# Performance work log

Measured on AMD Instinct MI355X. Metric: run time of the kernel, lower is better.

The kernel has to match this reference:

```python
import math
import jax, jax.numpy as jnp
import numpy as np

B, N, D, H, HID = 2, 2048, 1024, 16, 4096
KS = (7, 25, 49)

def _alibi_slopes(n):
    def p2(m):
        start = 2.0 ** (-(2.0 ** (-(math.log2(m) - 3))))
        return [start * (start ** i) for i in range(m)]
    if math.log2(n).is_integer():
        s = p2(n)
    else:
        cp2 = 2 ** int(math.floor(math.log2(n)))
        s = p2(cp2) + p2(2 * cp2)[0::2][: n - cp2]
    return jnp.asarray(s, dtype=jnp.float32)

def _ln(x, g, b, eps=1e-5):
    m = x.mean(-1, keepdims=True)
    v = ((x - m) ** 2).mean(-1, keepdims=True)
    return (x - m) / jnp.sqrt(v + eps) * g + b

def _dwconv(x, w, pl, pr, mode, bias=None):
    # x: (B, D, L) channels-first, w: (D, 1, k) depthwise kernel
    xp = jnp.pad(x, ((0, 0), (0, 0), (pl, pr)), mode=mode)
    y = jax.lax.conv_general_dilated(xp, w, (1,), 'VALID',
                                     dimension_numbers=('NCH', 'OIH', 'NCH'),
                                     feature_group_count=x.shape[1])
    if bias is not None:
        y = y + bias[None, :, None]
    return y

def _forward(x, periodic_bias, alpha, dw7, dw25, dw49, ln1_g, ln1_b, ln2_g, ln2_b,
             Wq, bq, Wk, bk, Wv, bv, Wo, bo, W1, b1, W2, b2, tw, tb):
    Bx, Nx, Dm = x.shape
    hd = Dm // H
    # --- series decomposition: softmax-weighted multi-scale moving averages ---
    xt = x.transpose(0, 2, 1)  # (B, D, N)
    branches = [_dwconv(xt, w, k // 2, k // 2, 'reflect')
                for w, k in ((dw7, 7), (dw25, 25), (dw49, 49))]
    wmix = jax.nn.softmax(alpha)
    T = sum(br * wi for br, wi in zip(branches, wmix)).transpose(0, 2, 1)  # trend (B,N,D)
    S = x - T  # seasonal
    # --- ALiBi self-attention on normalized seasonal part ---
    sn = _ln(S, ln1_g, ln1_b)
    q = (jnp.einsum('bnd,ed->bne', sn, Wq) + bq).reshape(Bx, Nx, H, hd)
    k = (jnp.einsum('bnd,ed->bne', sn, Wk) + bk).reshape(Bx, Nx, H, hd)
    v = (jnp.einsum('bnd,ed->bne', sn, Wv) + bv).reshape(Bx, Nx, H, hd)
    logits = jnp.einsum('bqhd,bkhd->bhqk', q, k) / np.float32(np.sqrt(hd))
    idx = jnp.arange(Nx)
    dist = jnp.maximum(idx[None, :] - idx[:, None], 0).astype(jnp.float32)  # clamp(j-i, 0)
    slopes = _alibi_slopes(H)
    logits = logits - slopes[None, :, None, None] * dist[None, None] + periodic_bias[None, None]
    attn = jax.nn.softmax(logits, axis=-1)
    o = jnp.einsum('bhqk,bkhd->bqhd', attn, v).reshape(Bx, Nx, Dm)
    y = jnp.einsum('bnd,ed->bne', o, Wo) + bo
    x_s = S + y
    # --- dense FFN (exact GELU, as torch nn.GELU default) ---
    h = _ln(x_s, ln2_g, ln2_b)
    ffn = jnp.einsum('bnh,dh->bnd',
                     jax.nn.gelu(jnp.einsum('bnd,hd->bnh', h, W1) + b1, approximate=False),
                     W2) + b2
    x_s = x_s + ffn
    # --- trend path: depthwise conv k=5, zero padding 2 ---
    t_out = _dwconv(T.transpose(0, 2, 1), tw, 2, 2, 'constant', tb).transpose(0, 2, 1)
    return x_s + t_out

def setup_inputs():
    key = jax.random.key(0)
    ks = jax.random.split(key, 12)
    def lin(k, o, i):
        return jax.random.normal(k, (o, i), jnp.float32) / np.float32(np.sqrt(i))
    return {
        'x': jax.random.normal(ks[0], (B, N, D), jnp.float32),
        'periodic_bias': 0.1 * jax.random.normal(ks[1], (N, N), jnp.float32),
        'alpha': jnp.zeros((len(KS),), jnp.float32),
        'dw7': jnp.full((D, 1, 7), 1.0 / 7, jnp.float32),
        'dw25': jnp.full((D, 1, 25), 1.0 / 25, jnp.float32),
        'dw49': jnp.full((D, 1, 49), 1.0 / 49, jnp.float32),
        'ln1_g': jnp.ones((D,), jnp.float32), 'ln1_b': jnp.zeros((D,), jnp.float32),
        'ln2_g': jnp.ones((D,), jnp.float32), 'ln2_b': jnp.zeros((D,), jnp.float32),
        'Wq': lin(ks[2], D, D), 'bq': jnp.zeros((D,), jnp.float32),
        'Wk': lin(ks[3], D, D), 'bk': jnp.zeros((D,), jnp.float32),
        'Wv': lin(ks[4], D, D), 'bv': jnp.zeros((D,), jnp.float32),
        'Wo': lin(ks[5], D, D), 'bo': jnp.zeros((D,), jnp.float32),
        'W1': lin(ks[6], HID, D), 'b1': jnp.zeros((HID,), jnp.float32),
        'W2': lin(ks[7], D, HID), 'b2': jnp.zeros((D,), jnp.float32),
        'tw': 0.1 * jax.random.normal(ks[8], (D, 1, 5), jnp.float32),
        'tb': jnp.zeros((D,), jnp.float32),
    }

def reference(x, periodic_bias, alpha, dw7, dw25, dw49, ln1_g, ln1_b, ln2_g, ln2_b,
              Wq, bq, Wk, bk, Wv, bv, Wo, bo, W1, b1, W2, b2, tw, tb):
    out = _forward(x, periodic_bias, alpha, dw7, dw25, dw49, ln1_g, ln1_b, ln2_g, ln2_b,
                   Wq, bq, Wk, bk, Wv, bv, Wo, bo, W1, b1, W2, b2, tw, tb)
    return (out, jnp.zeros((), out.dtype))
```

## Files before the change

kernel.cpp:

```cpp
#include <hip/hip_runtime.h>
#include <cstdint>

#define BB 2
#define NN 2048
#define DD 1024
#define HH 16
#define HD 64
#define HID_ 4096
#define MM (BB*NN)

typedef __bf16 bf16x8 __attribute__((ext_vector_type(8)));
typedef float  f32x4  __attribute__((ext_vector_type(4)));

__device__ inline void gload_lds16(const void* g, void* l) {
  __builtin_amdgcn_global_load_lds((const __attribute__((address_space(1))) char*)g,
                                   (__attribute__((address_space(3))) char*)l, 16, 0, 0);
}
__device__ inline float max3f(float a, float b, float c) { return fmaxf(fmaxf(a, b), c); }

__global__ void k_wcomb(const float* __restrict__ alpha, const float* __restrict__ dw7,
                        const float* __restrict__ dw25, const float* __restrict__ dw49,
                        float* __restrict__ wc,
                        const float* __restrict__ bq, const float* __restrict__ bk,
                        const float* __restrict__ bv, float* __restrict__ b3) {
  int t = blockIdx.x;
  if (t == 49) {
    for (int i = threadIdx.x; i < 3 * DD; i += blockDim.x) {
      const float* s = (i < DD) ? bq : (i < 2 * DD ? bk : bv);
      b3[i] = s[i & (DD - 1)];
    }
    return;
  }
  float a0 = alpha[0], a1 = alpha[1], a2 = alpha[2];
  float mx = fmaxf(a0, fmaxf(a1, a2));
  float e0 = __expf(a0 - mx), e1 = __expf(a1 - mx), e2 = __expf(a2 - mx);
  float inv = 1.f / (e0 + e1 + e2);
  float w0 = e0 * inv, w1 = e1 * inv, w2 = e2 * inv;
  for (int d = threadIdx.x; d < DD; d += blockDim.x) {
    float v = w2 * dw49[d * 49 + t];
    if (t >= 12 && t <= 36) v += w1 * dw25[d * 25 + (t - 12)];
    if (t >= 21 && t <= 27) v += w0 * dw7[d * 7 + (t - 21)];
    wc[t * DD + d] = v;
  }
}

__global__ __launch_bounds__(256) void k_cvtall(const float* __restrict__ Wq, const float* __restrict__ Wk,
                         const float* __restrict__ Wv, const float* __restrict__ Wo,
                         const float* __restrict__ W1, const float* __restrict__ W2,
                         __bf16* __restrict__ dst) {
  size_t i = ((size_t)blockIdx.x * 256 + threadIdx.x) * 4;
  const float* s;
  if (i < 1048576u) s = Wq + i;
  else if (i < 2097152u) s = Wk + (i - 1048576u);
  else if (i < 3145728u) s = Wv + (i - 2097152u);
  else if (i < 4194304u) s = Wo + (i - 3145728u);
  else if (i < 8388608u) s = W1 + (i - 4194304u);
  else s = W2 + (i - 8388608u);
  float4 v = *(const float4*)s;
  dst[i] = (__bf16)v.x; dst[i+1] = (__bf16)v.y; dst[i+2] = (__bf16)v.z; dst[i+3] = (__bf16)v.w;
}

__global__ __launch_bounds__(256) void k_pbt(const float* __restrict__ pb,
                                             __bf16* __restrict__ pbt) {
  int q = blockIdx.x;
  int qt16 = q >> 4, qm = q & 15;
  for (int k = threadIdx.x; k < NN; k += 256) {
    float v = pb[(size_t)q * NN + k] * 1.4426950408889634f;
    int kt = k >> 4, g = (k >> 2) & 3, rr = k & 3;
    pbt[((size_t)qt16 * 128 + kt) * 256 + (qm + 16 * g) * 4 + rr] = (__bf16)v;
  }
}

__global__ __launch_bounds__(256) void k_decomp(const float* __restrict__ x,
                                                const float* __restrict__ wc,
                                                const float* __restrict__ tw,
                                                const float* __restrict__ tb,
                                                float* __restrict__ S,
                                                float* __restrict__ tout) {
  int bid = blockIdx.x;
  int db = bid & 3, ns = (bid >> 2) & 127, b = bid >> 9;
  int d = db * 256 + threadIdx.x;
  int n0 = ns * 16;
  const float* xb = x + (size_t)b * NN * DD + d;
  float xw[68];
#pragma unroll
  for (int i = 0; i < 68; ++i) {
    int n = n0 - 26 + i;
    n = (n < 0) ? -n : n;
    n = (n > NN - 1) ? 2 * (NN - 1) - n : n;
    xw[i] = xb[(size_t)n * DD];
  }
  float Tx[20];
#pragma unroll
  for (int j = 0; j < 20; ++j) Tx[j] = 0.f;
#pragma unroll
  for (int t = 0; t < 49; ++t) {
    float wv = wc[t * DD + d];
#pragma unroll
    for (int j = 0; j < 20; ++j) Tx[j] = fmaf(wv, xw[j + t], Tx[j]);
  }
#pragma unroll
  for (int j = 0; j < 20; ++j) {
    int row = n0 - 2 + j;
    if (row < 0 || row >= NN) Tx[j] = 0.f;
  }
  float tw5[5];
#pragma unroll
  for (int t = 0; t < 5; ++t) tw5[t] = tw[d * 5 + t];
  float tbv = tb[d];
  size_t base = ((size_t)b * NN + n0) * DD + d;
#pragma unroll
  for (int i = 0; i < 16; ++i) {
    S[base + (size_t)i * DD] = xw[i + 26] - Tx[i + 2];
    float acc = tbv;
#pragma unroll
    for (int t = 0; t < 5; ++t) acc = fmaf(tw5[t], Tx[i + t], acc);
    tout[base + (size_t)i * DD] = acc;
  }
}

__global__ __launch_bounds__(256) void k_ln(const float* __restrict__ x,
                                            const float* __restrict__ g,
                                            const float* __restrict__ bt,
                                            __bf16* __restrict__ y) {
  int row = blockIdx.x;
  const float* xr = x + (size_t)row * DD;
  int i = threadIdx.x * 4;
  float4 v = *(const float4*)&xr[i];
  float s = v.x + v.y + v.z + v.w;
  float sq = v.x * v.x + v.y * v.y + v.z * v.z + v.w * v.w;
#pragma unroll
  for (int m = 1; m <= 32; m <<= 1) { s += __shfl_xor(s, m); sq += __shfl_xor(sq, m); }
  __shared__ float rs[4], rq[4];
  int wid = threadIdx.x >> 6;
  if ((threadIdx.x & 63) == 0) { rs[wid] = s; rq[wid] = sq; }
  __syncthreads();
  s = rs[0] + rs[1] + rs[2] + rs[3];
  sq = rq[0] + rq[1] + rq[2] + rq[3];
  float mean = s * (1.f / DD);
  float var = sq * (1.f / DD) - mean * mean;
  float rstd = rsqrtf(var + 1e-5f);
  float4 gv = *(const float4*)&g[i];
  float4 bv = *(const float4*)&bt[i];
  __bf16* yr = y + (size_t)row * DD + i;
  yr[0] = (__bf16)((v.x - mean) * rstd * gv.x + bv.x);
  yr[1] = (__bf16)((v.y - mean) * rstd * gv.y + bv.y);
  yr[2] = (__bf16)((v.z - mean) * rstd * gv.z + bv.z);
  yr[3] = (__bf16)((v.w - mean) * rstd * gv.w + bv.w);
}

template <int EPI, int BNT, int BKT>
__global__ __launch_bounds__(256) void k_gemm(const __bf16* __restrict__ A,
                                              const __bf16* __restrict__ Bw, int K,
                                              const float* __restrict__ bias,
                                              const float* __restrict__ aux1,
                                              const float* __restrict__ aux2,
                                              float* __restrict__ outf,
                                              __bf16* __restrict__ outb) {
  constexpr int NFR = BNT / 32;
  constexpr int NKK = BKT / 32;
  __shared__ __bf16 aS[2][128 * BKT];
  __shared__ __bf16 bS[2][BNT * BKT];
  const int tid = threadIdx.x;
  const int lane = tid & 63;
  const int wid = tid >> 6;
  const int wm = wid >> 1, wn = wid & 1;
  const int r = lane & 15, gq = lane >> 4;
  const int gx = gridDim.x;
  const int G = gx * gridDim.y;
  int bid = blockIdx.y * gx + blockIdx.x;
  int swz = (bid & 7) * (G >> 3) + (bid >> 3);
  const int m0 = (swz / gx) * 128;
  const int n0 = (swz % gx) * BNT;
  const int rsw = (BKT == 64) ? (r & 7) * 8 : 0;

  f32x4 acc[4][NFR];
#pragma unroll
  for (int mi = 0; mi < 4; ++mi)
#pragma unroll
    for (int ni = 0; ni < NFR; ++ni) acc[mi][ni] = (f32x4){0.f, 0.f, 0.f, 0.f};

  auto stage = [&](int bufi, int k0) {
#pragma unroll
    for (int i = 0; i < (128 * BKT) / 2048; ++i) {
      int e = i * 2048 + tid * 8;
      int row = e / BKT, col = e % BKT;
      int src = (BKT == 64) ? (col ^ ((row & 7) * 8)) : col;
      gload_lds16(A + (size_t)(m0 + row) * K + k0 + src, &aS[bufi][e]);
    }
#pragma unroll
    for (int i = 0; i < (BNT * BKT) / 2048; ++i) {
      int e = i * 2048 + tid * 8;
      int row = e / BKT, col = e % BKT;
      int src = (BKT == 64) ? (col ^ ((row & 7) * 8)) : col;
      gload_lds16(Bw + (size_t)(n0 + row) * K + k0 + src, &bS[bufi][e]);
    }
  };

  stage(0, 0);
  const int nk = K / BKT;
  int buf = 0;
  for (int kt = 0; kt < nk; ++kt) {
    __syncthreads();
    if (kt + 1 < nk) stage(buf ^ 1, (kt + 1) * BKT);
    bf16x8 af[4][NKK], bfr[NFR][NKK];
#pragma unroll
    for (int mi = 0; mi < 4; ++mi)
#pragma unroll
      for (int kk = 0; kk < NKK; ++kk)
        af[mi][kk] = *reinterpret_cast<const bf16x8*>(
            &aS[buf][(wm * 64 + mi * 16 + r) * BKT + ((kk * 32 + gq * 8) ^ rsw)]);
#pragma unroll
    for (int ni = 0; ni < NFR; ++ni)
#pragma unroll
      for (int kk = 0; kk < NKK; ++kk)
        bfr[ni][kk] = *reinterpret_cast<const bf16x8*>(
            &bS[buf][(wn * (BNT / 2) + ni * 16 + r) * BKT + ((kk * 32 + gq * 8) ^ rsw)]);
    __builtin_amdgcn_s_setprio(1);
#pragma unroll
    for (int kk = 0; kk < NKK; ++kk)
#pragma unroll
      for (int mi = 0; mi < 4; ++mi)
#pragma unroll
        for (int ni = 0; ni < NFR; ++ni)
          acc[mi][ni] = __builtin_amdgcn_mfma_f32_16x16x32_bf16(af[mi][kk], bfr[ni][kk], acc[mi][ni], 0, 0, 0);
    __builtin_amdgcn_s_setprio(0);
    buf ^= 1;
  }

#pragma unroll
  for (int mi = 0; mi < 4; ++mi) {
#pragma unroll
    for (int ni = 0; ni < NFR; ++ni) {
      int colg = n0 + wn * (BNT / 2) + ni * 16 + r;
      float bcol = bias[colg];
#pragma unroll
      for (int rr = 0; rr < 4; ++rr) {
        int mg = m0 + wm * 64 + mi * 16 + gq * 4 + rr;
        float val = acc[mi][ni][rr] + bcol;
        if constexpr (EPI == 0) {
          int which = colg >> 10, e = colg & 1023;
          int hh = e >> 6, d = e & 63;
          int b = mg >> 11, nq = mg & (NN - 1);
          if (which == 2) {
            int nl = nq & 63, kk = nl & 31;
            int slot = ((kk >> 4) << 2) | (((kk >> 2) & 3) << 3) | (kk & 3) | (nl & 32);
            int nqp = (nq & ~63) | slot;
            outb[(size_t)2 * (BB * HH * NN * HD) +
                 ((size_t)((b * HH + hh) * HD + d)) * NN + nqp] = (__bf16)val;
          } else {
            outb[(size_t)which * (BB * HH * NN * HD) +
                 ((size_t)(b * HH + hh) * NN + nq) * HD + d] = (__bf16)val;
          }
        } else if constexpr (EPI == 1) {
          size_t idx = (size_t)mg * DD + colg;
          outf[idx] = aux1[idx] + val;
        } else if constexpr (EPI == 2) {
          float gl = val * 0.5f * (1.f + erff(val * 0.70710678118f));
          outb[(size_t)mg * HID_ + colg] = (__bf16)gl;
        } else {
          size_t idx = (size_t)mg * DD + colg;
          outf[idx] = val + aux1[idx] + aux2[idx];
        }
      }
    }
  }
}

__global__ __launch_bounds__(512) void k_attn(const __bf16* __restrict__ qb,
                                              const __bf16* __restrict__ kb,
                                              const __bf16* __restrict__ vtb,
                                              const __bf16* __restrict__ pbt,
                                              __bf16* __restrict__ ob) {
  __shared__ __bf16 kS[2][64 * 64];
  __shared__ __bf16 vS[2][64 * 64];
  int blk = ((blockIdx.x & 7) << 6) | (blockIdx.x >> 3);
  int qt = blk & 15, bh = blk >> 4;
  int h = bh & (HH - 1), b = bh >> 4;
  int tid = threadIdx.x;
  int lane = tid & 63, w = tid >> 6;
  int r = lane & 15, g = lane >> 4;
  const __bf16* Kp = kb + (size_t)bh * NN * HD;
  const __bf16* Vt = vtb + (size_t)bh * HD * NN;
  int qbase = qt * 128 + w * 16;
  int cq = qt * 2 + (w >> 2);
  const __bf16* Q = qb + ((size_t)bh * NN + qbase) * HD;

  bf16x8 qf0 = *(const bf16x8*)&Q[(size_t)r * HD + g * 8];
  bf16x8 qf1 = *(const bf16x8*)&Q[(size_t)r * HD + 32 + g * 8];
  bf16x8 onesf;
#pragma unroll
  for (int j = 0; j < 8; ++j) onesf[j] = (__bf16)1.0f;

  const float C = 0.18033688011112042f;
  const float THRL2 = 11.541560327111707f;
  float slope = exp2f(-0.5f * (float)(h + 1)) * 1.4426950408889634f;
  float sconst[16];
#pragma unroll
  for (int st = 0; st < 4; ++st)
#pragma unroll
    for (int rr = 0; rr < 4; ++rr) sconst[st * 4 + rr] = slope * (float)(st * 16 + rr);
  float aL = slope * (float)(g * 4 - r);

  float m = 0.f;
  f32x4 oacc[4], lacc;
#pragma unroll
  for (int t = 0; t < 4; ++t) oacc[t] = (f32x4){0.f, 0.f, 0.f, 0.f};
  lacc = (f32x4){0.f, 0.f, 0.f, 0.f};

  auto stage = [&](int bufi, int kc0) {
    int row = tid >> 3;
    int c = (tid & 7) * 8;
    int src = c ^ ((row & 7) * 8);
    gload_lds16(Kp + (size_t)(kc0 + row) * HD + src, &kS[bufi][tid * 8]);
    gload_lds16(Vt + (size_t)row * NN + kc0 + src, &vS[bufi][tid * 8]);
  };

  stage(0, 0);
  int buf = 0;
  size_t tilebase = (size_t)(qt * 8 + w) * 128;
  int sw = (r & 7) * 8;

  for (int ch = 0; ch < NN / 64; ++ch) {
    int kc0 = ch * 64;
    __syncthreads();
    if (ch + 1 < NN / 64) stage(buf ^ 1, kc0 + 64);

    uint2 ub[4];
#pragma unroll
    for (int st = 0; st < 4; ++st)
      ub[st] = *(const uint2*)&pbt[(tilebase + (kc0 >> 4) + st) * 256 + lane * 4];

    f32x4 sacc[4];
    __builtin_amdgcn_s_setprio(1);
#pragma unroll
    for (int st = 0; st < 4; ++st) {
      sacc[st] = (f32x4){0.f, 0.f, 0.f, 0.f};
      int rowb = (st * 16 + r) * 64;
      bf16x8 kf0 = *(const bf16x8*)&kS[buf][rowb + ((g * 8) ^ sw)];
      bf16x8 kf1 = *(const bf16x8*)&kS[buf][rowb + ((32 + g * 8) ^ sw)];
      sacc[st] = __builtin_amdgcn_mfma_f32_16x16x32_bf16(kf0, qf0, sacc[st], 0, 0, 0);
      sacc[st] = __builtin_amdgcn_mfma_f32_16x16x32_bf16(kf1, qf1, sacc[st], 0, 0, 0);
    }
    __builtin_amdgcn_s_setprio(0);

    float zm[16];
    if (ch > cq) {
      float uu = fmaf(slope, (float)(kc0 - qbase), aL) + m;
#pragma unroll
      for (int st = 0; st < 4; ++st) {
        float p0 = __uint_as_float(ub[st].x << 16);
        float p1 = __uint_as_float(ub[st].x & 0xffff0000u);
        float p2 = __uint_as_float(ub[st].y << 16);
        float p3 = __uint_as_float(ub[st].y & 0xffff0000u);
        zm[st*4+0] = fmaf(sacc[st][0], C, p0) - uu - sconst[st*4+0];
        zm[st*4+1] = fmaf(sacc[st][1], C, p1) - uu - sconst[st*4+1];
        zm[st*4+2] = fmaf(sacc[st][2], C, p2) - uu - sconst[st*4+2];
        zm[st*4+3] = fmaf(sacc[st][3], C, p3) - uu - sconst[st*4+3];
      }
    } else if (ch < cq) {
#pragma unroll
      for (int st = 0; st < 4; ++st) {
        float p0 = __uint_as_float(ub[st].x << 16);
        float p1 = __uint_as_float(ub[st].x & 0xffff0000u);
        float p2 = __uint_as_float(ub[st].y << 16);
        float p3 = __uint_as_float(ub[st].y & 0xffff0000u);
        zm[st*4+0] = fmaf(sacc[st][0], C, p0) - m;
        zm[st*4+1] = fmaf(sacc[st][1], C, p1) - m;
        zm[st*4+2] = fmaf(sacc[st][2], C, p2) - m;
        zm[st*4+3] = fmaf(sacc[st][3], C, p3) - m;
      }
    } else {
      int kqb = kc0 + g * 4 - qbase - r;
#pragma unroll
      for (int st = 0; st < 4; ++st) {
        float p0 = __uint_as_float(ub[st].x << 16);
        float p1 = __uint_as_float(ub[st].x & 0xffff0000u);
        float p2 = __uint_as_float(ub[st].y << 16);
        float p3 = __uint_as_float(ub[st].y & 0xffff0000u);
        float pb4[4] = {p0, p1, p2, p3};
#pragma unroll
        for (int rr = 0; rr < 4; ++rr) {
          int dk = kqb + st * 16 + rr;
          float dist = (dk > 0) ? (float)dk : 0.f;
          zm[st*4+rr] = fmaf(sacc[st][rr], C, pb4[rr]) - fmaf(slope, dist, m);
        }
      }
    }

    float l0 = max3f(zm[0], zm[1], zm[2]);
    float l1 = max3f(zm[3], zm[4], zm[5]);
    float l2 = max3f(zm[6], zm[7], zm[8]);
    float l3 = max3f(zm[9], zm[10], zm[11]);
    float l4 = max3f(zm[12], zm[13], zm[14]);
    float zmax = fmaxf(max3f(l0, l1, l2), max3f(l3, l4, zm[15]));
    if (__any(zmax > THRL2)) {
      float rowmax = fmaxf(zmax, __shfl_xor(zmax, 16));
      rowmax = fmaxf(rowmax, __shfl_xor(rowmax, 32));
      float delta = fmaxf(rowmax, 0.f);
      m += delta;
      float sc = exp2f(-delta);
      float sco[4];
#pragma unroll
      for (int rr = 0; rr < 4; ++rr) sco[rr] = __shfl(sc, g * 4 + rr);
#pragma unroll
      for (int rr = 0; rr < 4; ++rr) {
        lacc[rr] *= sco[rr];
#pragma unroll
        for (int t = 0; t < 4; ++t) oacc[t][rr] *= sco[rr];
      }
#pragma unroll
      for (int j = 0; j < 16; ++j) zm[j] -= delta;
    }

    bf16x8 pa0, pa1;
#pragma unroll
    for (int j = 0; j < 8; ++j) {
      pa0[j] = (__bf16)exp2f(zm[(j >> 2) * 4 + (j & 3)]);
      pa1[j] = (__bf16)exp2f(zm[(2 + (j >> 2)) * 4 + (j & 3)]);
    }

    __builtin_amdgcn_s_setprio(1);
#pragma unroll
    for (int t = 0; t < 4; ++t) {
      int rowb = (t * 16 + r) * 64;
      bf16x8 vf0 = *(const bf16x8*)&vS[buf][rowb + ((g * 8) ^ sw)];
      bf16x8 vf1 = *(const bf16x8*)&vS[buf][rowb + ((32 + g * 8) ^ sw)];
      oacc[t] = __builtin_amdgcn_mfma_f32_16x16x32_bf16(pa0, vf0, oacc[t], 0, 0, 0);
      oacc[t] = __builtin_amdgcn_mfma_f32_16x16x32_bf16(pa1, vf1, oacc[t], 0, 0, 0);
    }
    lacc = __builtin_amdgcn_mfma_f32_16x16x32_bf16(pa0, onesf, lacc, 0, 0, 0);
    lacc = __builtin_amdgcn_mfma_f32_16x16x32_bf16(pa1, onesf, lacc, 0, 0, 0);
    __builtin_amdgcn_s_setprio(0);
    buf ^= 1;
  }

#pragma unroll
  for (int rr = 0; rr < 4; ++rr) {
    int qg = qbase + g * 4 + rr;
    float inv = 1.f / lacc[rr];
#pragma unroll
    for (int t = 0; t < 4; ++t) {
      float v = oacc[t][rr] * inv;
      ob[((size_t)(b * NN) + qg) * DD + h * HD + t * 16 + r] = (__bf16)v;
    }
  }
}

__global__ void k_tail(float* __restrict__ out) { out[(size_t)BB * NN * DD] = 0.f; }

extern "C" void kernel_launch(void* const* d_in, const int* in_sizes, int n_in,
                              void* d_out, int out_size, void* d_ws, size_t ws_size,
                              hipStream_t stream) {
  const float* x    = (const float*)d_in[0];
  const float* pb   = (const float*)d_in[1];
  const float* alpha= (const float*)d_in[2];
  const float* dw7  = (const float*)d_in[3];
  const float* dw25 = (const float*)d_in[4];
  const float* dw49 = (const float*)d_in[5];
  const float* ln1g = (const float*)d_in[6];
  const float* ln1b = (const float*)d_in[7];
  const float* ln2g = (const float*)d_in[8];
  const float* ln2b = (const float*)d_in[9];
  const float* Wq   = (const float*)d_in[10];
  const float* bq   = (const float*)d_in[11];
  const float* Wk   = (const float*)d_in[12];
  const float* bk   = (const float*)d_in[13];
  const float* Wv   = (const float*)d_in[14];
  const float* bv   = (const float*)d_in[15];
  const float* Wo   = (const float*)d_in[16];
  const float* bo   = (const float*)d_in[17];
  const float* W1   = (const float*)d_in[18];
  const float* b1   = (const float*)d_in[19];
  const float* W2   = (const float*)d_in[20];
  const float* b2   = (const float*)d_in[21];
  const float* tw   = (const float*)d_in[22];
  const float* tb   = (const float*)d_in[23];
  float* out = (float*)d_out;

  char* w = (char*)d_ws;
  size_t off = 0;
  auto alloc = [&](size_t bytes) -> char* {
    char* p = w + off;
    off = (off + bytes + 255) & ~(size_t)255;
    return p;
  };
  float*  wc    = (float*)alloc(49 * 1024 * 4);
  float*  b3    = (float*)alloc(3072 * 4);
  float*  Tbuf  = (float*)alloc((size_t)MM * DD * 4);
  float*  Sbuf  = (float*)alloc((size_t)MM * DD * 4);
  float*  toutb = (float*)alloc((size_t)MM * DD * 4);
  __bf16* sn    = (__bf16*)alloc((size_t)MM * DD * 2);
  __bf16* qkv   = (__bf16*)alloc((size_t)3 * MM * DD * 2);
  __bf16* gb    = (__bf16*)alloc((size_t)MM * HID_ * 2);
  __bf16* wall  = (__bf16*)alloc((size_t)12582912 * 2);
  __bf16* pbt   = (__bf16*)alloc((size_t)NN * NN * 2);
  __bf16* wqkvb = wall;
  __bf16* wob   = wall + (size_t)3 * DD * DD;
  __bf16* w1b   = wall + (size_t)4 * DD * DD;
  __bf16* w2b   = wall + (size_t)4 * DD * DD + (size_t)HID_ * DD;
  float*  xs    = Tbuf;
  __bf16* obuf  = sn;
  __bf16* hb    = qkv;

  const size_t BHND = (size_t)BB * HH * NN * HD;

  k_wcomb<<<50, 256, 0, stream>>>(alpha, dw7, dw25, dw49, wc, bq, bk, bv, b3);
  k_pbt<<<NN, 256, 0, stream>>>(pb, pbt);
  k_cvtall<<<12288, 256, 0, stream>>>(Wq, Wk, Wv, Wo, W1, W2, wall);
  k_decomp<<<1024, 256, 0, stream>>>(x, wc, tw, tb, Sbuf, toutb);
  k_ln<<<MM, 256, 0, stream>>>(Sbuf, ln1g, ln1b, sn);
  k_gemm<0,128,32><<<dim3(24, 32), 256, 0, stream>>>(sn, wqkvb, DD, b3, nullptr, nullptr, nullptr, qkv);
  k_attn<<<BB * HH * (NN / 128), 512, 0, stream>>>(qkv, qkv + BHND, qkv + 2 * BHND, pbt, obuf);
  k_gemm<1,64,64><<<dim3(16, 32), 256, 0, stream>>>(obuf, wob, DD, bo, Sbuf, nullptr, xs, nullptr);
  k_ln<<<MM, 256, 0, stream>>>(xs, ln2g, ln2b, hb);
  k_gemm<2,128,64><<<dim3(32, 32), 256, 0, stream>>>(hb, w1b, DD, b1, nullptr, nullptr, nullptr, gb);
  k_gemm<3,64,64><<<dim3(16, 32), 256, 0, stream>>>(gb, w2b, HID_, b2, xs, toutb, out, nullptr);
  k_tail<<<1, 1, 0, stream>>>(out);
}
```

Measured before the change: 310.3 us.

## Store seasonal and trend intermediates in bf16, pack attention math, widen QKV K-tile

The decomposition kernel now writes the seasonal part S and the trend-conv output as bf16 instead of fp32. The LayerNorm and GEMM epilogues read these through new bf16 paths, which halves the memory traffic for these intermediates. The attention softmax preprocessing is rewritten with packed float2 vectors so it can use packed FP32 ops. The QKV GEMM K-tile is raised from 32 to 64. The residual adds now use bf16-rounded S and trend values, which loses some accuracy.

```diff
diff --git a/kernel.cpp b/kernel.cpp
--- a/kernel.cpp
+++ b/kernel.cpp
@@ -10,7 +10,9 @@
 #define MM (BB*NN)
 
 typedef __bf16 bf16x8 __attribute__((ext_vector_type(8)));
+typedef __bf16 bf16x4 __attribute__((ext_vector_type(4)));
 typedef float  f32x4  __attribute__((ext_vector_type(4)));
+typedef float  f32x2  __attribute__((ext_vector_type(2)));
 
 __device__ inline void gload_lds16(const void* g, void* l) {
   __builtin_amdgcn_global_load_lds((const __attribute__((address_space(1))) char*)g,
@@ -75,8 +77,8 @@
                                                 const float* __restrict__ wc,
                                                 const float* __restrict__ tw,
                                                 const float* __restrict__ tb,
-                                                float* __restrict__ S,
-                                                float* __restrict__ tout) {
+                                                __bf16* __restrict__ S,
+                                                __bf16* __restrict__ tout) {
   int bid = blockIdx.x;
   int db = bid & 3, ns = (bid >> 2) & 127, b = bid >> 9;
   int d = db * 256 + threadIdx.x;
@@ -111,22 +113,28 @@
   size_t base = ((size_t)b * NN + n0) * DD + d;
 #pragma unroll
   for (int i = 0; i < 16; ++i) {
-    S[base + (size_t)i * DD] = xw[i + 26] - Tx[i + 2];
+    S[base + (size_t)i * DD] = (__bf16)(xw[i + 26] - Tx[i + 2]);
     float acc = tbv;
 #pragma unroll
     for (int t = 0; t < 5; ++t) acc = fmaf(tw5[t], Tx[i + t], acc);
-    tout[base + (size_t)i * DD] = acc;
-  }
-}
-
-__global__ __launch_bounds__(256) void k_ln(const float* __restrict__ x,
+    tout[base + (size_t)i * DD] = (__bf16)acc;
+  }
+}
+
+template <int INBF>
+__global__ __launch_bounds__(256) void k_ln(const void* __restrict__ xv,
                                             const float* __restrict__ g,
                                             const float* __restrict__ bt,
                                             __bf16* __restrict__ y) {
   int row = blockIdx.x;
-  const float* xr = x + (size_t)row * DD;
   int i = threadIdx.x * 4;
-  float4 v = *(const float4*)&xr[i];
+  float4 v;
+  if constexpr (INBF) {
+    bf16x4 x4 = *(const bf16x4*)((const __bf16*)xv + (size_t)row * DD + i);
+    v.x = (float)x4[0]; v.y = (float)x4[1]; v.z = (float)x4[2]; v.w = (float)x4[3];
+  } else {
+    v = *(const float4*)((const float*)xv + (size_t)row * DD + i);
+  }
   float s = v.x + v.y + v.z + v.w;
   float sq = v.x * v.x + v.y * v.y + v.z * v.z + v.w * v.w;
 #pragma unroll
@@ -153,8 +161,8 @@
 __global__ __launch_bounds__(256) void k_gemm(const __bf16* __restrict__ A,
                                               const __bf16* __restrict__ Bw, int K,
                                               const float* __restrict__ bias,
-                                              const float* __restrict__ aux1,
-                                              const float* __restrict__ aux2,
+                                              const float* __restrict__ auxf,
+                                              const __bf16* __restrict__ auxb,
                                               float* __restrict__ outf,
                                               __bf16* __restrict__ outb) {
   constexpr int NFR = BNT / 32;
@@ -254,13 +262,13 @@
           }
         } else if constexpr (EPI == 1) {
           size_t idx = (size_t)mg * DD + colg;
-          outf[idx] = aux1[idx] + val;
+          outf[idx] = (float)auxb[idx] + val;
         } else if constexpr (EPI == 2) {
           float gl = val * 0.5f * (1.f + erff(val * 0.70710678118f));
           outb[(size_t)mg * HID_ + colg] = (__bf16)gl;
         } else {
           size_t idx = (size_t)mg * DD + colg;
-          outf[idx] = val + aux1[idx] + aux2[idx];
+          outf[idx] = val + auxf[idx] + (float)auxb[idx];
         }
       }
     }
@@ -293,13 +301,15 @@
   for (int j = 0; j < 8; ++j) onesf[j] = (__bf16)1.0f;
 
   const float C = 0.18033688011112042f;
+  const f32x2 C2 = {C, C};
   const float THRL2 = 11.541560327111707f;
   float slope = exp2f(-0.5f * (float)(h + 1)) * 1.4426950408889634f;
-  float sconst[16];
-#pragma unroll
-  for (int st = 0; st < 4; ++st)
-#pragma unroll
-    for (int rr = 0; rr < 4; ++rr) sconst[st * 4 + rr] = slope * (float)(st * 16 + rr);
+  f32x2 sconst2[8];
+#pragma unroll
+  for (int st = 0; st < 4; ++st) {
+    sconst2[st * 2]     = (f32x2){slope * (float)(st * 16),     slope * (float)(st * 16 + 1)};
+    sconst2[st * 2 + 1] = (f32x2){slope * (float)(st * 16 + 2), slope * (float)(st * 16 + 3)};
+  }
   float aL = slope * (float)(g * 4 - r);
 
   float m = 0.f;
@@ -344,31 +354,29 @@
     }
     __builtin_amdgcn_s_setprio(0);
 
-    float zm[16];
+    f32x2 z2[8];
     if (ch > cq) {
       float uu = fmaf(slope, (float)(kc0 - qbase), aL) + m;
+      f32x2 uu2 = {uu, uu};
 #pragma unroll
       for (int st = 0; st < 4; ++st) {
-        float p0 = __uint_as_float(ub[st].x << 16);
-        float p1 = __uint_as_float(ub[st].x & 0xffff0000u);
-        float p2 = __uint_as_float(ub[st].y << 16);
-        float p3 = __uint_as_float(ub[st].y & 0xffff0000u);
-        zm[st*4+0] = fmaf(sacc[st][0], C, p0) - uu - sconst[st*4+0];
-        zm[st*4+1] = fmaf(sacc[st][1], C, p1) - uu - sconst[st*4+1];
-        zm[st*4+2] = fmaf(sacc[st][2], C, p2) - uu - sconst[st*4+2];
-        zm[st*4+3] = fmaf(sacc[st][3], C, p3) - uu - sconst[st*4+3];
+        f32x2 pbl = {__uint_as_float(ub[st].x << 16), __uint_as_float(ub[st].x & 0xffff0000u)};
+        f32x2 pbh = {__uint_as_float(ub[st].y << 16), __uint_as_float(ub[st].y & 0xffff0000u)};
+        f32x2 s0 = {sacc[st][0], sacc[st][1]};
+        f32x2 s1 = {sacc[st][2], sacc[st][3]};
+        z2[st*2]   = s0 * C2 + pbl - (uu2 + sconst2[st*2]);
+        z2[st*2+1] = s1 * C2 + pbh - (uu2 + sconst2[st*2+1]);
       }
     } else if (ch < cq) {
+      f32x2 m2 = {m, m};
 #pragma unroll
       for (int st = 0; st < 4; ++st) {
-        float p0 = __uint_as_float(ub[st].x << 16);
-        float p1 = __uint_as_float(ub[st].x & 0xffff0000u);
-        float p2 = __uint_as_float(ub[st].y << 16);
-        float p3 = __uint_as_float(ub[st].y & 0xffff0000u);
-        zm[st*4+0] = fmaf(sacc[st][0], C, p0) - m;
-        zm[st*4+1] = fmaf(sacc[st][1], C, p1) - m;
-        zm[st*4+2] = fmaf(sacc[st][2], C, p2) - m;
-        zm[st*4+3] = fmaf(sacc[st][3], C, p3) - m;
+        f32x2 pbl = {__uint_as_float(ub[st].x << 16), __uint_as_float(ub[st].x & 0xffff0000u)};
+        f32x2 pbh = {__uint_as_float(ub[st].y << 16), __uint_as_float(ub[st].y & 0xffff0000u)};
+        f32x2 s0 = {sacc[st][0], sacc[st][1]};
+        f32x2 s1 = {sacc[st][2], sacc[st][3]};
+        z2[st*2]   = s0 * C2 + pbl - m2;
+        z2[st*2+1] = s1 * C2 + pbh - m2;
       }
     } else {
       int kqb = kc0 + g * 4 - qbase - r;
@@ -383,17 +391,18 @@
         for (int rr = 0; rr < 4; ++rr) {
           int dk = kqb + st * 16 + rr;
           float dist = (dk > 0) ? (float)dk : 0.f;
-          zm[st*4+rr] = fmaf(sacc[st][rr], C, pb4[rr]) - fmaf(slope, dist, m);
+          z2[st*2 + (rr >> 1)][rr & 1] =
+              fmaf(sacc[st][rr], C, pb4[rr]) - fmaf(slope, dist, m);
         }
       }
     }
 
-    float l0 = max3f(zm[0], zm[1], zm[2]);
-    float l1 = max3f(zm[3], zm[4], zm[5]);
-    float l2 = max3f(zm[6], zm[7], zm[8]);
-    float l3 = max3f(zm[9], zm[10], zm[11]);
-    float l4 = max3f(zm[12], zm[13], zm[14]);
-    float zmax = fmaxf(max3f(l0, l1, l2), max3f(l3, l4, zm[15]));
+    float l0 = max3f(z2[0][0], z2[0][1], z2[1][0]);
+    float l1 = max3f(z2[1][1], z2[2][0], z2[2][1]);
+    float l2 = max3f(z2[3][0], z2[3][1], z2[4][0]);
+    float l3 = max3f(z2[4][1], z2[5][0], z2[5][1]);
+    float l4 = max3f(z2[6][0], z2[6][1], z2[7][0]);
+    float zmax = fmaxf(max3f(l0, l1, l2), max3f(l3, l4, z2[7][1]));
     if (__any(zmax > THRL2)) {
       float rowmax = fmaxf(zmax, __shfl_xor(zmax, 16));
       rowmax = fmaxf(rowmax, __shfl_xor(rowmax, 32));
@@ -409,15 +418,16 @@
 #pragma unroll
         for (int t = 0; t < 4; ++t) oacc[t][rr] *= sco[rr];
       }
-#pragma unroll
-      for (int j = 0; j < 16; ++j) zm[j] -= delta;
+      f32x2 d2 = {delta, delta};
+#pragma unroll
+      for (int j = 0; j < 8; ++j) z2[j] -= d2;
     }
 
     bf16x8 pa0, pa1;
 #pragma unroll
     for (int j = 0; j < 8; ++j) {
-      pa0[j] = (__bf16)exp2f(zm[(j >> 2) * 4 + (j & 3)]);
-      pa1[j] = (__bf16)exp2f(zm[(2 + (j >> 2)) * 4 + (j & 3)]);
+      pa0[j] = (__bf16)exp2f(z2[j >> 1][j & 1]);
+      pa1[j] = (__bf16)exp2f(z2[4 + (j >> 1)][j & 1]);
     }
 
     __builtin_amdgcn_s_setprio(1);
@@ -487,9 +497,9 @@
   };
   float*  wc    = (float*)alloc(49 * 1024 * 4);
   float*  b3    = (float*)alloc(3072 * 4);
-  float*  Tbuf  = (float*)alloc((size_t)MM * DD * 4);
-  float*  Sbuf  = (float*)alloc((size_t)MM * DD * 4);
-  float*  toutb = (float*)alloc((size_t)MM * DD * 4);
+  float*  xs    = (float*)alloc((size_t)MM * DD * 4);
+  __bf16* Sb    = (__bf16*)alloc((size_t)MM * DD * 2);
+  __bf16* toutb = (__bf16*)alloc((size_t)MM * DD * 2);
   __bf16* sn    = (__bf16*)alloc((size_t)MM * DD * 2);
   __bf16* qkv   = (__bf16*)alloc((size_t)3 * MM * DD * 2);
   __bf16* gb    = (__bf16*)alloc((size_t)MM * HID_ * 2);
@@ -499,7 +509,6 @@
   __bf16* wob   = wall + (size_t)3 * DD * DD;
   __bf16* w1b   = wall + (size_t)4 * DD * DD;
   __bf16* w2b   = wall + (size_t)4 * DD * DD + (size_t)HID_ * DD;
-  float*  xs    = Tbuf;
   __bf16* obuf  = sn;
   __bf16* hb    = qkv;
 
@@ -508,12 +517,12 @@
   k_wcomb<<<50, 256, 0, stream>>>(alpha, dw7, dw25, dw49, wc, bq, bk, bv, b3);
   k_pbt<<<NN, 256, 0, stream>>>(pb, pbt);
   k_cvtall<<<12288, 256, 0, stream>>>(Wq, Wk, Wv, Wo, W1, W2, wall);
-  k_decomp<<<1024, 256, 0, stream>>>(x, wc, tw, tb, Sbuf, toutb);
-  k_ln<<<MM, 256, 0, stream>>>(Sbuf, ln1g, ln1b, sn);
-  k_gemm<0,128,32><<<dim3(24, 32), 256, 0, stream>>>(sn, wqkvb, DD, b3, nullptr, nullptr, nullptr, qkv);
+  k_decomp<<<1024, 256, 0, stream>>>(x, wc, tw, tb, Sb, toutb);
+  k_ln<1><<<MM, 256, 0, stream>>>(Sb, ln1g, ln1b, sn);
+  k_gemm<0,128,64><<<dim3(24, 32), 256, 0, stream>>>(sn, wqkvb, DD, b3, nullptr, nullptr, nullptr, qkv);
   k_attn<<<BB * HH * (NN / 128), 512, 0, stream>>>(qkv, qkv + BHND, qkv + 2 * BHND, pbt, obuf);
-  k_gemm<1,64,64><<<dim3(16, 32), 256, 0, stream>>>(obuf, wob, DD, bo, Sbuf, nullptr, xs, nullptr);
-  k_ln<<<MM, 256, 0, stream>>>(xs, ln2g, ln2b, hb);
+  k_gemm<1,64,64><<<dim3(16, 32), 256, 0, stream>>>(obuf, wob, DD, bo, nullptr, Sb, xs, nullptr);
+  k_ln<0><<<MM, 256, 0, stream>>>(xs, ln2g, ln2b, hb);
   k_gemm<2,128,64><<<dim3(32, 32), 256, 0, stream>>>(hb, w1b, DD, b1, nullptr, nullptr, nullptr, gb);
   k_gemm<3,64,64><<<dim3(16, 32), 256, 0, stream>>>(gb, w2b, HID_, b2, xs, toutb, out, nullptr);
   k_tail<<<1, 1, 0, stream>>>(out);
```

Result: slower. 320.0 us (+3.1%).
